# Kernel tuning notes

Hardware: AMD Instinct MI355X
Metric: run time of the kernel (lower is better)

The kernel has to match this reference:

```python
import jax, jax.numpy as jnp
import numpy as np

B, T, NB, D, E = 2, 4096, 4, 512, 4096
TEMP = 1.0
CAP_F = 1.5
NOISE_KEY = 42


def setup_inputs() -> dict:
    key = jax.random.key(0)
    k1, k2 = jax.random.split(key)
    x = jax.random.normal(k1, (B, T, NB * D), dtype=jnp.float32)
    # Tied weights: embedding_table[i].weight is embedding_decoder[i].weight, shape [E, D] per block
    W = jax.random.normal(k2, (NB, E, D), dtype=jnp.float32) * 0.02
    return {"x": x, "W": W}


def reference(x, W):
    Bv, Tv, _ = x.shape
    xb = x.reshape(Bv, Tv, NB, D)
    expert_capacity = int(Bv * Tv / E * CAP_F)  # = 3 here
    # per-block decoder logits: [B, T, NB, E]
    dist_logits = jnp.einsum('btnd,ned->btne', xb, W)
    # noise = 1 - temperature * rand_like(logits)
    noise = 1.0 - TEMP * jax.random.uniform(jax.random.key(NOISE_KEY), dist_logits.shape, dtype=dist_logits.dtype)
    noisy = dist_logits * noise
    # top-k over the token axis T (dim=1 in torch) per (b, block, element)
    nt = noisy.transpose(0, 2, 3, 1)  # [B, NB, E, T]
    _, topk_idx = jax.lax.top_k(nt, expert_capacity)  # [B, NB, E, k]
    mask = jnp.zeros(nt.shape, dtype=bool)
    bI = jnp.arange(Bv)[:, None, None, None]
    nI = jnp.arange(NB)[None, :, None, None]
    eI = jnp.arange(E)[None, None, :, None]
    mask = mask.at[bI, nI, eI, topk_idx].set(True)
    maskf = mask.transpose(0, 3, 1, 2).astype(noisy.dtype)  # [B, T, NB, E]
    # argmax over codebook dim of masked noisy logits
    decoded_indices = jnp.argmax(maskf * noisy, axis=-1)  # [B, T, NB]
    # embedding gather with tied table W[n]: [B, T, NB, D]
    latents = jax.vmap(lambda w, i: w[i], in_axes=(0, 2), out_axes=2)(W, decoded_indices)
    decoded_latents = latents.reshape(Bv, Tv, NB * D)  # cat along dim=2
    return decoded_indices, decoded_latents, dist_logits
```

## Files before the change

kernel.cpp:

```cpp
#include <hip/hip_runtime.h>
#include <stdint.h>

#define B_     2
#define T_     4096
#define NB_    4
#define D_     512
#define E_     4096
#define NE_    16384
#define HALF_  67108864u
#define SLOTS_ 32768
#define XN8_   2097152
#define WN8_   1048576
#define MT_    32
#define RECN_  (64 * NE_)

typedef unsigned long long u64;
typedef uint32_t u32;
typedef uint16_t u16;
typedef _Float16 f16x8 __attribute__((ext_vector_type(8)));
typedef float    f32x4 __attribute__((ext_vector_type(4)));

__device__ __forceinline__ u32 rotl32(u32 x, int r) { return __builtin_rotateleft32(x, r); }

__device__ __forceinline__ void tf_0_42(u32 x0, u32 x1, u32 &o0, u32 &o1) {
  const u32 ks0 = 0u, ks1 = 42u, ks2 = 0x1BD11BDAu ^ 0u ^ 42u;
  x0 += ks0; x1 += ks1;
#define TFR(r) { x0 += x1; x1 = rotl32(x1, (r)); x1 ^= x0; }
  TFR(13) TFR(15) TFR(26) TFR(6)
  x0 += ks1; x1 += ks2 + 1u;
  TFR(17) TFR(29) TFR(16) TFR(24)
  x0 += ks2; x1 += ks0 + 2u;
  TFR(13) TFR(15) TFR(26) TFR(6)
  x0 += ks0; x1 += ks1 + 3u;
  TFR(17) TFR(29) TFR(16) TFR(24)
  x0 += ks1; x1 += ks2 + 4u;
  TFR(13) TFR(15) TFR(26) TFR(6)
  x0 += ks2; x1 += ks0 + 5u;
#undef TFR
  o0 = x0; o1 = x1;
}

__device__ __forceinline__ float noise_at(u32 i) {
  u32 o0, o1; tf_0_42(0u, i, o0, o1);
  u32 bits = o0 ^ o1;
  float f = __uint_as_float((bits >> 9) | 0x3F800000u);
  return 2.0f - f;
}

__device__ __forceinline__ u32 map_f32(float v) {
  u32 u = __float_as_uint(v);
  u32 s = (u32)((int)u >> 31);
  return u ^ (s | 0x80000000u);
}

__device__ __forceinline__ void merge3(u64 &a0, u64 &a1, u64 &a2,
                                       u64 b0, u64 b1, u64 b2) {
  u64 o0, o1, o2;
  if (a0 >= b0) {
    o0 = a0;
    if (a1 >= b0) { o1 = a1; o2 = (a2 >= b0) ? a2 : b0; }
    else          { o1 = b0; o2 = (a1 >= b1) ? a1 : b1; }
  } else {
    o0 = b0;
    if (b1 >= a0) { o1 = b1; o2 = (b2 >= a0) ? b2 : a0; }
    else          { o1 = a0; o2 = (b1 >= a1) ? b1 : a1; }
  }
  a0 = o0; a1 = o1; a2 = o2;
}

#define BASE_KEY 0x80000000FFFFFFFFull
#define SCALE_   2048.0f
#define INV_SC   (1.0f / 4194304.0f)

__global__ __launch_bounds__(256) void init_keys(u64* __restrict__ keys,
                                                 u32* __restrict__ thr) {
  int i = blockIdx.x * 256 + threadIdx.x;
  keys[i] = BASE_KEY;
  thr[i]  = 0u;
}

__device__ __forceinline__ void split8v(const float4 a0, const float4 a1, f16x8 &hi, f16x8 &lo) {
  float fv[8] = {a0.x, a0.y, a0.z, a0.w, a1.x, a1.y, a1.z, a1.w};
#pragma unroll
  for (int j = 0; j < 8; ++j) {
    float f = fv[j] * SCALE_;
    _Float16 h = (_Float16)f;
    hi[j] = h;
    lo[j] = (_Float16)(f - (float)h);
  }
}

__global__ __launch_bounds__(256) void presplit(const float* __restrict__ x,
                                                const float* __restrict__ W,
                                                f16x8* __restrict__ xh, f16x8* __restrict__ xl,
                                                f16x8* __restrict__ wh, f16x8* __restrict__ wl) {
  size_t g = (size_t)blockIdx.x * 256 + threadIdx.x;
  const float4* src;
  f16x8 *dh, *dl;
  size_t off;
  if (g < XN8_) { src = (const float4*)x; dh = xh; dl = xl; off = g; }
  else          { src = (const float4*)W; dh = wh; dl = wl; off = g - XN8_; }
  float4 a0 = src[off * 2], a1 = src[off * 2 + 1];
  f16x8 hi, lo;
  split8v(a0, a1, hi, lo);
  dh[off] = hi; dl[off] = lo;
}

#define BM 128
#define BN 128

__global__ __launch_bounds__(256) void gemm_fused(const f16x8* __restrict__ xh,
                                                  const f16x8* __restrict__ xl,
                                                  const f16x8* __restrict__ wh,
                                                  const f16x8* __restrict__ wl,
                                                  float* __restrict__ logits,
                                                  u64* __restrict__ k0g,
                                                  u64* __restrict__ k1g,
                                                  u64* __restrict__ k2g,
                                                  u32* __restrict__ thrbuf) {
  __shared__ f16x8 lds_raw[2048];
  f16x8* AhV = lds_raw;
  f16x8* AlV = lds_raw + 512;
  f16x8* BhV = lds_raw + 1024;
  f16x8* BlV = lds_raw + 1536;

  const int id = blockIdx.x;
  const int e0 = (id & 31) * BN;
  const int n  = (id >> 5) & 3;
  const int mt = id >> 7;
  const int m0 = mt * BM;

  const int tid  = threadIdx.x;
  const int lane = tid & 63;
  const int wid  = tid >> 6;
  const int wr   = wid >> 1;
  const int wc   = wid & 1;
  const int lm   = lane & 15;
  const int lk   = lane >> 4;

  f32x4 acc[4][4];
#pragma unroll
  for (int i = 0; i < 4; ++i)
#pragma unroll
    for (int j = 0; j < 4; ++j) acc[i][j] = (f32x4){0.f, 0.f, 0.f, 0.f};

  for (int k0 = 0; k0 < D_ / 8; k0 += 4) {
#pragma unroll
    for (int l = 0; l < 2; ++l) {
      int aid = tid + l * 256;
      int r   = aid >> 2;
      int ko  = aid & 3;
      int ps  = ko ^ ((r >> 1) & 3);
      size_t gA = ((size_t)(m0 + r) * NB_ + n) * (D_ / 8) + k0 + ko;
      AhV[r * 4 + ps] = xh[gA];
      AlV[r * 4 + ps] = xl[gA];
      size_t gB = ((size_t)n * E_ + e0 + r) * (D_ / 8) + k0 + ko;
      BhV[r * 4 + ps] = wh[gB];
      BlV[r * 4 + ps] = wl[gB];
    }
    __syncthreads();

    f16x8 bh[4], bl[4];
#pragma unroll
    for (int fn = 0; fn < 4; ++fn) {
      int row = wc * 64 + fn * 16 + lm;
      int ps  = lk ^ ((row >> 1) & 3);
      bh[fn] = BhV[row * 4 + ps];
      bl[fn] = BlV[row * 4 + ps];
    }
#pragma unroll
    for (int fm = 0; fm < 4; ++fm) {
      int row = wr * 64 + fm * 16 + lm;
      int ps  = lk ^ ((row >> 1) & 3);
      f16x8 ah = AhV[row * 4 + ps];
      f16x8 al = AlV[row * 4 + ps];
#pragma unroll
      for (int fn = 0; fn < 4; ++fn) {
        acc[fm][fn] = __builtin_amdgcn_mfma_f32_16x16x32_f16(ah, bh[fn], acc[fm][fn], 0, 0, 0);
        acc[fm][fn] = __builtin_amdgcn_mfma_f32_16x16x32_f16(ah, bl[fn], acc[fm][fn], 0, 0, 0);
        acc[fm][fn] = __builtin_amdgcn_mfma_f32_16x16x32_f16(al, bh[fn], acc[fm][fn], 0, 0, 0);
      }
    }
    __syncthreads();
  }
  float* lgbuf = (float*)lds_raw;
  u16*   tbuf  = (u16*)((char*)lds_raw + 16384);
  u64*   ldsK  = (u64*)((char*)lds_raw + 24576);

  const int b     = m0 >> 12;
  const int mbase = m0 & (T_ - 1);
  const int mtile = mbase >> 7;

#pragma unroll
  for (int fm = 0; fm < 4; ++fm) {
#pragma unroll
    for (int r = 0; r < 4; ++r) {
      int m = m0 + wr * 64 + fm * 16 + lk * 4 + r;
      float* row = logits + ((size_t)m * NB_ + n) * E_ + e0 + wc * 64 + lm;
#pragma unroll
      for (int fn = 0; fn < 4; ++fn) row[fn * 16] = acc[fm][fn][r] * INV_SC;
    }
  }

#pragma unroll
  for (int fn = 0; fn < 4; ++fn) {
    const int e  = e0 + wc * 64 + fn * 16 + lm;
    const int ne = n * E_ + e;
    const u32 thrv = thrbuf[(size_t)b * NE_ + ne];

    int cnt = 0;
#pragma unroll
    for (int fm = 0; fm < 4; ++fm) {
#pragma unroll
      for (int r = 0; r < 4; ++r) {
        float lg = acc[fm][fn][r] * INV_SC;
        u32 mu = __float_as_uint(fmaxf(lg, 0.0f)) | 0x80000000u;
        if (mu >= thrv) {
          lgbuf[cnt * 256 + tid] = lg;
          tbuf [cnt * 256 + tid] = (u16)(mbase + wr * 64 + fm * 16 + lk * 4 + r);
          ++cnt;
        }
      }
    }

    u32 v0 = 0, v1 = 0, v2 = 0;
    u32 tt0 = 0, tt1 = 0, tt2 = 0;
    const u32 ibase = (u32)b * HALF_ + (u32)ne;
    for (int k = 0; k < cnt; ++k) {
      float lg = lgbuf[k * 256 + tid];
      u32 t    = (u32)tbuf[k * 256 + tid];
      float y  = lg * noise_at(ibase + t * (u32)NE_);
      u32 mv = map_f32(y);
      bool g0 = mv > v0, g1 = mv > v1, g2 = mv > v2;
      v2  = g1 ? v1  : (g2 ? mv : v2);
      tt2 = g1 ? tt1 : (g2 ? t  : tt2);
      v1  = g0 ? v0  : (g1 ? mv : v1);
      tt1 = g0 ? tt0 : (g1 ? t  : tt1);
      v0  = g0 ? mv  : v0;
      tt0 = g0 ? t   : tt0;
    }

    u64 K0 = ((u64)v0 << 32) | (u64)(0xFFFFFFFFu - tt0);
    u64 K1 = ((u64)v1 << 32) | (u64)(0xFFFFFFFFu - tt1);
    u64 K2 = ((u64)v2 << 32) | (u64)(0xFFFFFFFFu - tt2);
    u64 p0 = __shfl_xor(K0, 16), p1 = __shfl_xor(K1, 16), p2 = __shfl_xor(K2, 16);
    merge3(K0, K1, K2, p0, p1, p2);
    p0 = __shfl_xor(K0, 32); p1 = __shfl_xor(K1, 32); p2 = __shfl_xor(K2, 32);
    merge3(K0, K1, K2, p0, p1, p2);
    if (lk == 0) {
      int c = fn * 16 + lm;
      ldsK[(wid * 64 + c) * 3 + 0] = K0;
      ldsK[(wid * 64 + c) * 3 + 1] = K1;
      ldsK[(wid * 64 + c) * 3 + 2] = K2;
    }
  }
  __syncthreads();
  if (wid < 2) {
    int c = lane;
    u64 A0 = ldsK[(wid * 64 + c) * 3 + 0];
    u64 A1 = ldsK[(wid * 64 + c) * 3 + 1];
    u64 A2 = ldsK[(wid * 64 + c) * 3 + 2];
    u64 C0 = ldsK[((wid + 2) * 64 + c) * 3 + 0];
    u64 C1 = ldsK[((wid + 2) * 64 + c) * 3 + 1];
    u64 C2 = ldsK[((wid + 2) * 64 + c) * 3 + 2];
    merge3(A0, A1, A2, C0, C1, C2);
    int eg = e0 + wid * 64 + c;
    size_t R = (size_t)(mtile * 2 + b) * NE_ + (size_t)n * E_ + eg;
    k0g[R] = A0; k1g[R] = A1; k2g[R] = A2;
    atomicMax(&thrbuf[(size_t)b * NE_ + (size_t)n * E_ + eg], (u32)(A2 >> 32));
  }
}

__global__ __launch_bounds__(256) void merge_scatter2(const u64* __restrict__ k0g,
                                                      const u64* __restrict__ k1g,
                                                      const u64* __restrict__ k2g,
                                                      u64* __restrict__ keys) {
  int gid2 = blockIdx.x * 256 + threadIdx.x;
  int b  = gid2 >> 14;
  int ne = gid2 & (NE_ - 1);

  u64 K0 = 0, K1 = 0, K2 = 0;
  for (int mt = 0; mt < MT_; ++mt) {
    size_t R = (size_t)(mt * 2 + b) * NE_ + ne;
    merge3(K0, K1, K2, k0g[R], k1g[R], k2g[R]);
  }

  int n = ne >> 12;
  u32 e = (u32)(ne & (E_ - 1));
  u64 elo = (u64)(0xFFFFFFFFu - e);
  u32 t0 = 0xFFFFFFFFu - (u32)K0;
  u32 t1 = 0xFFFFFFFFu - (u32)K1;
  u32 t2 = 0xFFFFFFFFu - (u32)K2;
  atomicMax(&keys[((size_t)b * T_ + t0) * NB_ + n], (K0 & 0xFFFFFFFF00000000ull) | elo);
  atomicMax(&keys[((size_t)b * T_ + t1) * NB_ + n], (K1 & 0xFFFFFFFF00000000ull) | elo);
  atomicMax(&keys[((size_t)b * T_ + t2) * NB_ + n], (K2 & 0xFFFFFFFF00000000ull) | elo);
}

__device__ __forceinline__ void split8(const float* __restrict__ p, f16x8 &hi, f16x8 &lo) {
  float4 a0 = *(const float4*)p;
  float4 a1 = *(const float4*)(p + 4);
  split8v(a0, a1, hi, lo);
}

__global__ __launch_bounds__(256) void gemm_logits_fb(const float* __restrict__ x,
                                                      const float* __restrict__ W,
                                                      float* __restrict__ logits) {
  __shared__ f16x8 AhV[128 * 4];
  __shared__ f16x8 AlV[128 * 4];
  __shared__ f16x8 BhV[128 * 4];
  __shared__ f16x8 BlV[128 * 4];

  const int n  = blockIdx.z;
  const int m0 = blockIdx.y * BM;
  const int e0 = blockIdx.x * BN;
  const int tid  = threadIdx.x;
  const int lane = tid & 63;
  const int wid  = tid >> 6;
  const int wr   = wid >> 1;
  const int wc   = wid & 1;
  const int lm   = lane & 15;
  const int lk   = lane >> 4;

  const float* Abase = x + ((size_t)m0 * NB_ + n) * D_;
  const float* Bbase = W + ((size_t)n * E_ + e0) * D_;

  f32x4 acc[4][4];
#pragma unroll
  for (int i = 0; i < 4; ++i)
#pragma unroll
    for (int j = 0; j < 4; ++j) acc[i][j] = (f32x4){0.f, 0.f, 0.f, 0.f};

  for (int k0 = 0; k0 < D_; k0 += 32) {
#pragma unroll
    for (int l = 0; l < 2; ++l) {
      int aid = tid + l * 256;
      int r   = aid >> 2;
      int ko  = aid & 3;
      int ps  = ko ^ ((r >> 1) & 3);
      f16x8 hi, lo;
      split8(Abase + (size_t)r * (NB_ * D_) + k0 + ko * 8, hi, lo);
      AhV[r * 4 + ps] = hi; AlV[r * 4 + ps] = lo;
      split8(Bbase + (size_t)r * D_ + k0 + ko * 8, hi, lo);
      BhV[r * 4 + ps] = hi; BlV[r * 4 + ps] = lo;
    }
    __syncthreads();

    f16x8 bh[4], bl[4];
#pragma unroll
    for (int fn = 0; fn < 4; ++fn) {
      int row = wc * 64 + fn * 16 + lm;
      int ps  = lk ^ ((row >> 1) & 3);
      bh[fn] = BhV[row * 4 + ps];
      bl[fn] = BlV[row * 4 + ps];
    }
#pragma unroll
    for (int fm = 0; fm < 4; ++fm) {
      int row = wr * 64 + fm * 16 + lm;
      int ps  = lk ^ ((row >> 1) & 3);
      f16x8 ah = AhV[row * 4 + ps];
      f16x8 al = AlV[row * 4 + ps];
#pragma unroll
      for (int fn = 0; fn < 4; ++fn) {
        acc[fm][fn] = __builtin_amdgcn_mfma_f32_16x16x32_f16(ah, bh[fn], acc[fm][fn], 0, 0, 0);
        acc[fm][fn] = __builtin_amdgcn_mfma_f32_16x16x32_f16(ah, bl[fn], acc[fm][fn], 0, 0, 0);
        acc[fm][fn] = __builtin_amdgcn_mfma_f32_16x16x32_f16(al, bh[fn], acc[fm][fn], 0, 0, 0);
      }
    }
    __syncthreads();
  }

#pragma unroll
  for (int fm = 0; fm < 4; ++fm) {
#pragma unroll
    for (int fn = 0; fn < 4; ++fn) {
#pragma unroll
      for (int r = 0; r < 4; ++r) {
        int m = m0 + wr * 64 + fm * 16 + lk * 4 + r;
        int e = e0 + wc * 64 + fn * 16 + lm;
        logits[((size_t)m * NB_ + n) * E_ + e] = acc[fm][fn][r] * INV_SC;
      }
    }
  }
}

__global__ __launch_bounds__(256) void select_scatter(const float* __restrict__ logits,
                                                      u64* __restrict__ keys) {
  int gid = blockIdx.x * 256 + threadIdx.x;
  int b  = gid >> 14;
  int ne = gid & (NE_ - 1);

  float v0 = -1e30f, v1 = -1e30f, v2 = -1e30f;
  int   t0 = 0, t1 = 0, t2 = 0;

  const float* lg = logits + (size_t)b * HALF_;
  const u32 ib = (u32)b * HALF_ + (u32)ne;
  for (int t = 0; t < T_; ++t) {
    u32 i0 = (u32)t * (u32)NE_ + (u32)ne;
    float y = lg[i0] * noise_at(ib + (u32)t * (u32)NE_);
    if (y > v0)      { v2=v1; t2=t1; v1=v0; t1=t0; v0=y; t0=t; }
    else if (y > v1) { v2=v1; t2=t1; v1=y;  t1=t; }
    else if (y > v2) { v2=y;  t2=t; }
  }

  int n = ne >> 12;
  int e = ne & (E_ - 1);
  u64 klo = 0xFFFFFFFFull - (u32)e;
  atomicMax(&keys[((size_t)b * T_ + t0) * NB_ + n], ((u64)map_f32(v0) << 32) | klo);
  atomicMax(&keys[((size_t)b * T_ + t1) * NB_ + n], ((u64)map_f32(v1) << 32) | klo);
  atomicMax(&keys[((size_t)b * T_ + t2) * NB_ + n], ((u64)map_f32(v2) << 32) | klo);
}

__global__ __launch_bounds__(128) void finalize(const u64* __restrict__ keys,
                                                const float* __restrict__ W,
                                                float* __restrict__ out_idx,
                                                float* __restrict__ out_lat) {
  int slot = blockIdx.x;
  int n = slot & (NB_ - 1);
  int e = (int)(0xFFFFFFFFu - (u32)keys[slot]) & (E_ - 1);
  if (threadIdx.x == 0) out_idx[slot] = (float)e;

  const float4 v = ((const float4*)(W + ((size_t)n * E_ + e) * D_))[threadIdx.x];
  ((float4*)(out_lat + (size_t)slot * D_))[threadIdx.x] = v;
}

extern "C" void kernel_launch(void* const* d_in, const int* in_sizes, int n_in,
                              void* d_out, int out_size, void* d_ws, size_t ws_size,
                              hipStream_t stream) {
  const float* x = (const float*)d_in[0];
  const float* W = (const float*)d_in[1];

  float* out_idx    = (float*)d_out;
  float* out_lat    = out_idx + (size_t)SLOTS_;
  float* out_logits = out_lat + (size_t)SLOTS_ * D_;

  u64* keys = (u64*)d_ws;
  const size_t KEYS_B = (size_t)SLOTS_ * 8;
  const size_t THR_B  = (size_t)SLOTS_ * 4;
  const size_t XH_B   = (size_t)XN8_ * 16;
  const size_t WH_B   = (size_t)WN8_ * 16;
  bool split = ws_size >= KEYS_B + THR_B + 2 * XH_B + 2 * WH_B;

  u32*   thr = (u32*)((char*)d_ws + KEYS_B);
  char*  sp  = (char*)d_ws + KEYS_B + THR_B;
  f16x8* xh  = (f16x8*)sp;
  f16x8* xl  = (f16x8*)(sp + XH_B);
  f16x8* wh  = (f16x8*)(sp + 2 * XH_B);
  f16x8* wl  = (f16x8*)(sp + 2 * XH_B + WH_B);

  u64* k0g = (u64*)out_lat;
  u64* k1g = k0g + RECN_;
  u64* k2g = k1g + RECN_;

  init_keys<<<SLOTS_ / 256, 256, 0, stream>>>(keys, thr);

  if (split) {
    presplit<<<(XN8_ + WN8_) / 256, 256, 0, stream>>>(x, W, xh, xl, wh, wl);
    gemm_fused<<<8192, 256, 0, stream>>>(xh, xl, wh, wl, out_logits, k0g, k1g, k2g, thr);
    merge_scatter2<<<SLOTS_ / 256, 256, 0, stream>>>(k0g, k1g, k2g, keys);
  } else {
    dim3 ggrid(E_ / BN, (B_ * T_) / BM, NB_);
    gemm_logits_fb<<<ggrid, 256, 0, stream>>>(x, W, out_logits);
    select_scatter<<<SLOTS_ / 256, 256, 0, stream>>>(out_logits, keys);
  }

  finalize<<<SLOTS_, 128, 0, stream>>>(keys, W, out_idx, out_lat);
}
```

Baseline: 699.0 us.

## Presample strided token subset to seed per-column top-3 thresholds before main GEMM

Adds a small GEMM kernel over every 32nd token that computes noisy logits, keeps a per-(batch, block, code) top-3, and writes the third-best value into the threshold buffer. The main fused GEMM can then skip noise generation and candidate insertion for most elements from the start, instead of relying on thresholds that only tighten as it goes. It also reorders the main grid's block index so the block dimension is outermost, which changes cache reuse of the W tiles. The cost is an extra launch and roughly 1/32 extra GEMM work; correctness depends on the threshold being a valid lower bound, which holds since these are real samples.

```diff
diff --git a/kernel.cpp b/kernel.cpp
--- a/kernel.cpp
+++ b/kernel.cpp
@@ -109,6 +109,133 @@
 #define BM 128
 #define BN 128
 
+__global__ __launch_bounds__(256) void gemm_presample(const f16x8* __restrict__ xh,
+                                                      const f16x8* __restrict__ xl,
+                                                      const f16x8* __restrict__ wh,
+                                                      const f16x8* __restrict__ wl,
+                                                      u32* __restrict__ thrbuf) {
+  __shared__ f16x8 lds_raw[2048];
+  f16x8* AhV = lds_raw;
+  f16x8* AlV = lds_raw + 512;
+  f16x8* BhV = lds_raw + 1024;
+  f16x8* BlV = lds_raw + 1536;
+
+  const int id = blockIdx.x;
+  const int e0 = (id & 31) * BN;
+  const int n  = (id >> 5) & 3;
+  const int b  = id >> 7;
+
+  const int tid  = threadIdx.x;
+  const int lane = tid & 63;
+  const int wid  = tid >> 6;
+  const int wr   = wid >> 1;
+  const int wc   = wid & 1;
+  const int lm   = lane & 15;
+  const int lk   = lane >> 4;
+
+  f32x4 acc[4][4];
+#pragma unroll
+  for (int i = 0; i < 4; ++i)
+#pragma unroll
+    for (int j = 0; j < 4; ++j) acc[i][j] = (f32x4){0.f, 0.f, 0.f, 0.f};
+
+  for (int k0 = 0; k0 < D_ / 8; k0 += 4) {
+#pragma unroll
+    for (int l = 0; l < 2; ++l) {
+      int aid = tid + l * 256;
+      int r   = aid >> 2;
+      int ko  = aid & 3;
+      int ps  = ko ^ ((r >> 1) & 3);
+      size_t gA = ((size_t)(b * T_ + 32 * r) * NB_ + n) * (D_ / 8) + k0 + ko;
+      AhV[r * 4 + ps] = xh[gA];
+      AlV[r * 4 + ps] = xl[gA];
+      size_t gB = ((size_t)n * E_ + e0 + r) * (D_ / 8) + k0 + ko;
+      BhV[r * 4 + ps] = wh[gB];
+      BlV[r * 4 + ps] = wl[gB];
+    }
+    __syncthreads();
+
+    f16x8 bh[4], bl[4];
+#pragma unroll
+    for (int fn = 0; fn < 4; ++fn) {
+      int row = wc * 64 + fn * 16 + lm;
+      int ps  = lk ^ ((row >> 1) & 3);
+      bh[fn] = BhV[row * 4 + ps];
+      bl[fn] = BlV[row * 4 + ps];
+    }
+#pragma unroll
+    for (int fm = 0; fm < 4; ++fm) {
+      int row = wr * 64 + fm * 16 + lm;
+      int ps  = lk ^ ((row >> 1) & 3);
+      f16x8 ah = AhV[row * 4 + ps];
+      f16x8 al = AlV[row * 4 + ps];
+#pragma unroll
+      for (int fn = 0; fn < 4; ++fn) {
+        acc[fm][fn] = __builtin_amdgcn_mfma_f32_16x16x32_f16(ah, bh[fn], acc[fm][fn], 0, 0, 0);
+        acc[fm][fn] = __builtin_amdgcn_mfma_f32_16x16x32_f16(ah, bl[fn], acc[fm][fn], 0, 0, 0);
+        acc[fm][fn] = __builtin_amdgcn_mfma_f32_16x16x32_f16(al, bh[fn], acc[fm][fn], 0, 0, 0);
+      }
+    }
+    __syncthreads();
+  }
+  u64* ldsK = (u64*)lds_raw;
+
+#pragma unroll
+  for (int fn = 0; fn < 4; ++fn) {
+    const int e  = e0 + wc * 64 + fn * 16 + lm;
+    const int ne = n * E_ + e;
+    u32 v0 = 0, v1 = 0, v2 = 0;
+    u32 tt0 = 0, tt1 = 0, tt2 = 0;
+    const u32 ibase = (u32)b * HALF_ + (u32)ne;
+#pragma unroll
+    for (int fm = 0; fm < 4; ++fm) {
+#pragma unroll
+      for (int r = 0; r < 4; ++r) {
+        const u32 t = 32u * (u32)(wr * 64 + fm * 16 + lk * 4 + r);
+        float lg = acc[fm][fn][r] * INV_SC;
+        u32 mu = __float_as_uint(fmaxf(lg, 0.0f)) | 0x80000000u;
+        if (mu > v2) {
+          float y = lg * noise_at(ibase + t * (u32)NE_);
+          u32 mv = map_f32(y);
+          bool g0 = mv > v0, g1 = mv > v1, g2 = mv > v2;
+          v2  = g1 ? v1  : (g2 ? mv : v2);
+          tt2 = g1 ? tt1 : (g2 ? t  : tt2);
+          v1  = g0 ? v0  : (g1 ? mv : v1);
+          tt1 = g0 ? tt0 : (g1 ? t  : tt1);
+          v0  = g0 ? mv  : v0;
+          tt0 = g0 ? t   : tt0;
+        }
+      }
+    }
+    u64 K0 = ((u64)v0 << 32) | (u64)(0xFFFFFFFFu - tt0);
+    u64 K1 = ((u64)v1 << 32) | (u64)(0xFFFFFFFFu - tt1);
+    u64 K2 = ((u64)v2 << 32) | (u64)(0xFFFFFFFFu - tt2);
+    u64 p0 = __shfl_xor(K0, 16), p1 = __shfl_xor(K1, 16), p2 = __shfl_xor(K2, 16);
+    merge3(K0, K1, K2, p0, p1, p2);
+    p0 = __shfl_xor(K0, 32); p1 = __shfl_xor(K1, 32); p2 = __shfl_xor(K2, 32);
+    merge3(K0, K1, K2, p0, p1, p2);
+    if (lk == 0) {
+      int c = fn * 16 + lm;
+      ldsK[(wid * 64 + c) * 3 + 0] = K0;
+      ldsK[(wid * 64 + c) * 3 + 1] = K1;
+      ldsK[(wid * 64 + c) * 3 + 2] = K2;
+    }
+  }
+  __syncthreads();
+  if (wid < 2) {
+    int c = lane;
+    u64 A0 = ldsK[(wid * 64 + c) * 3 + 0];
+    u64 A1 = ldsK[(wid * 64 + c) * 3 + 1];
+    u64 A2 = ldsK[(wid * 64 + c) * 3 + 2];
+    merge3(A0, A1, A2,
+           ldsK[((wid + 2) * 64 + c) * 3 + 0],
+           ldsK[((wid + 2) * 64 + c) * 3 + 1],
+           ldsK[((wid + 2) * 64 + c) * 3 + 2]);
+    int eg = e0 + wid * 64 + c;
+    thrbuf[(size_t)b * NE_ + (size_t)n * E_ + eg] = (u32)(A2 >> 32);
+  }
+}
+
 __global__ __launch_bounds__(256) void gemm_fused(const f16x8* __restrict__ xh,
                                                   const f16x8* __restrict__ xl,
                                                   const f16x8* __restrict__ wh,
@@ -126,8 +253,8 @@
 
   const int id = blockIdx.x;
   const int e0 = (id & 31) * BN;
-  const int n  = (id >> 5) & 3;
-  const int mt = id >> 7;
+  const int mt = (id >> 5) & 63;
+  const int n  = id >> 11;
   const int m0 = mt * BM;
 
   const int tid  = threadIdx.x;
@@ -455,6 +582,7 @@
 
   if (split) {
     presplit<<<(XN8_ + WN8_) / 256, 256, 0, stream>>>(x, W, xh, xl, wh, wl);
+    gemm_presample<<<256, 256, 0, stream>>>(xh, xl, wh, wl, thr);
     gemm_fused<<<8192, 256, 0, stream>>>(xh, xl, wh, wl, out_logits, k0g, k1g, k2g, thr);
     merge_scatter2<<<SLOTS_ / 256, 256, 0, stream>>>(k0g, k1g, k2g, keys);
   } else {
```

Result: no change. 710.1 us (+1.6%).
